# Kernel tuning notes

Hardware: AMD Instinct MI355X
Metric: run time of the kernel (lower is better)

## Reference

```python
import jax, jax.numpy as jnp
import numpy as np

N, E, D, H = 50000, 800000, 128, 8
HD = D // H  # head dim = 16


def setup_inputs() -> dict:
    key = jax.random.key(0)
    ks = jax.random.split(key, 9)
    x = jax.random.normal(ks[0], (N, D), dtype=jnp.float32)
    edge_index = jax.random.randint(ks[1], (2, E), 0, N, dtype=jnp.int64)
    s = 0.05
    Wq = jax.random.normal(ks[2], (D, D), dtype=jnp.float32) * s
    bq = jax.random.normal(ks[3], (D,), dtype=jnp.float32) * s
    Wk = jax.random.normal(ks[4], (D, D), dtype=jnp.float32) * s
    bk = jax.random.normal(ks[5], (D,), dtype=jnp.float32) * s
    Wv = jax.random.normal(ks[6], (D, D), dtype=jnp.float32) * s
    bv = jax.random.normal(ks[7], (D,), dtype=jnp.float32) * s
    return {"x": x, "Wq": Wq, "bq": bq, "Wk": Wk, "bk": bk, "Wv": Wv, "bv": bv,
            "edge_index": edge_index}


def reference(x, Wq, bq, Wk, bk, Wv, bv, edge_index):
    n = x.shape[0]
    # Linear projections (torch Linear: x @ W.T + b), split into heads
    Q = (x @ Wq.T + bq).reshape(n, H, HD)  # [N,H,hd]
    K = (x @ Wk.T + bk).reshape(n, H, HD)
    V = (x @ Wv.T + bv).reshape(n, H, HD)
    src, dst = edge_index[0], edge_index[1]
    # per-edge attention score: sum over head dim of K[src]*Q[dst]/sqrt(hd), clamp, exp
    score = jnp.sum(K[src] * Q[dst], axis=-1, keepdims=True) / np.sqrt(HD)  # [E,H,1]
    score = jnp.exp(jnp.clip(score, -5.0, 5.0))
    msg = V[src] * score  # [E,H,hd]
    wV = jax.ops.segment_sum(msg, dst, num_segments=n)      # [N,H,hd]
    Z = jax.ops.segment_sum(score, dst, num_segments=n)     # [N,H,1]
    h_out = wV / (Z + 1e-6)
    return h_out.reshape(n, H * HD)
```

## Files before the change

### kernel.cpp

```cpp
#include <hip/hip_runtime.h>
#include <hip/hip_bf16.h>

#define NN 50000
#define EE 800000
#define DD 128
#define HH 8
#define CAP 64
#define KVS 256
#define QB 391
#define PAB 196
#define NBIN 196
#define RSTRIDE 4096

typedef short bf16x8 __attribute__((ext_vector_type(8)));
typedef float f32x4 __attribute__((ext_vector_type(4)));
typedef unsigned short ushort8_t __attribute__((ext_vector_type(8)));

__device__ __forceinline__ unsigned short f2b(float f) {
    unsigned int u = __builtin_bit_cast(unsigned int, f);
    unsigned int r = (u + 0x7FFFu + ((u >> 16) & 1u)) >> 16;
    return (unsigned short)r;
}
__device__ __forceinline__ float b2f(unsigned short u) {
    return __builtin_bit_cast(float, ((unsigned int)u) << 16);
}

__global__ __launch_bounds__(256) void prep(const float* __restrict__ Wq,
                                            const float* __restrict__ Wk,
                                            const float* __restrict__ Wv,
                                            unsigned short* __restrict__ Wqb,
                                            unsigned short* __restrict__ Wkb,
                                            unsigned short* __restrict__ Wvb) {
    int idx = blockIdx.x * 256 + threadIdx.x;
    int mat = idx >> 12;
    int off = idx & 4095;
    const float* src = (mat == 0) ? Wq : (mat == 1) ? Wk : Wv;
    unsigned short* dst = (mat == 0) ? Wqb : (mat == 1) ? Wkb : Wvb;
    float4 v = ((const float4*)src)[off];
    ushort4 o;
    o.x = f2b(v.x); o.y = f2b(v.y); o.z = f2b(v.z); o.w = f2b(v.w);
    ((ushort4*)dst)[off] = o;
}

template <int OUTKIND>
__device__ __forceinline__ void qkv_mat(const unsigned short* __restrict__ W,
                                        const float* __restrict__ bias,
                                        float* __restrict__ qo,
                                        unsigned short* __restrict__ kvo,
                                        int kvoff,
                                        const bf16x8 a[2][4],
                                        int r0, int mrow, int kb,
                                        bool act0, bool act1) {
#pragma unroll
    for (int c0 = 0; c0 < 8; ++c0) {
        float bval = bias[c0 * 16 + mrow];
        const unsigned short* wr = W + (size_t)(c0 * 16 + mrow) * DD + kb * 8;
        bf16x8 w0 = *(const bf16x8*)(wr);
        bf16x8 w1 = *(const bf16x8*)(wr + 32);
        bf16x8 w2 = *(const bf16x8*)(wr + 64);
        bf16x8 w3 = *(const bf16x8*)(wr + 96);
#pragma unroll
        for (int g = 0; g < 2; ++g) {
            bool act = (g == 0) ? act0 : act1;
            f32x4 acc = {bval, bval, bval, bval};
            acc = __builtin_amdgcn_mfma_f32_16x16x32_bf16(a[g][0], w0, acc, 0, 0, 0);
            acc = __builtin_amdgcn_mfma_f32_16x16x32_bf16(a[g][1], w1, acc, 0, 0, 0);
            acc = __builtin_amdgcn_mfma_f32_16x16x32_bf16(a[g][2], w2, acc, 0, 0, 0);
            acc = __builtin_amdgcn_mfma_f32_16x16x32_bf16(a[g][3], w3, acc, 0, 0, 0);
            if (act) {
                int orow = r0 + 16 * g + kb * 4;
                int col = c0 * 16 + mrow;
                if (OUTKIND == 0) {
#pragma unroll
                    for (int r = 0; r < 4; ++r)
                        qo[(size_t)(orow + r) * DD + col] = acc[r];
                } else {
#pragma unroll
                    for (int r = 0; r < 4; ++r)
                        kvo[(size_t)(orow + r) * KVS + kvoff + col] = f2b(acc[r]);
                }
            }
        }
    }
}

__global__ __launch_bounds__(256) void mega(
    const float* __restrict__ x,
    const unsigned short* __restrict__ Wq, const float* __restrict__ bq,
    const unsigned short* __restrict__ Wk, const float* __restrict__ bk,
    const unsigned short* __restrict__ Wv, const float* __restrict__ bv,
    const int* __restrict__ ei,
    float* __restrict__ Qo, unsigned short* __restrict__ KV,
    int2* __restrict__ runbuf, int* __restrict__ gcount,
    int* __restrict__ gstart) {
    __shared__ int lcnt[256];
    __shared__ int lpre[256];
    if (blockIdx.x < QB) {
        const int wave = threadIdx.x >> 6;
        const int l = threadIdx.x & 63;
        const int r0 = blockIdx.x * 128 + wave * 32;
        const int mrow = l & 15;
        const int kb = l >> 4;
        const bool act0 = (r0 < NN);
        const bool act1 = (r0 + 16 < NN);
        if (!act0) return;

        bf16x8 a[2][4];
#pragma unroll
        for (int g = 0; g < 2; ++g) {
            int row = (g == 0 || act1) ? (r0 + 16 * g + mrow) : r0;
            const float* xr = x + (size_t)row * DD + kb * 8;
#pragma unroll
            for (int s = 0; s < 4; ++s) {
                float4 f0 = *(const float4*)(xr + s * 32);
                float4 f1 = *(const float4*)(xr + s * 32 + 4);
                bf16x8 t;
                t[0] = (short)f2b(f0.x); t[1] = (short)f2b(f0.y);
                t[2] = (short)f2b(f0.z); t[3] = (short)f2b(f0.w);
                t[4] = (short)f2b(f1.x); t[5] = (short)f2b(f1.y);
                t[6] = (short)f2b(f1.z); t[7] = (short)f2b(f1.w);
                a[g][s] = t;
            }
        }
        qkv_mat<0>(Wq, bq, Qo, (unsigned short*)nullptr, 0, a, r0, mrow, kb, act0, act1);
        qkv_mat<1>(Wk, bk, (float*)nullptr, KV, 0,   a, r0, mrow, kb, act0, act1);
        qkv_mat<1>(Wv, bv, (float*)nullptr, KV, 128, a, r0, mrow, kb, act0, act1);
    } else {
        const int b = blockIdx.x - QB;
        const int t = threadIdx.x;
        lcnt[t] = 0;
        __syncthreads();

        int ss[16], dd[16], slot[16];
        int base4 = b * 1024 + t;
#pragma unroll
        for (int j = 0; j < 4; ++j) {
            int idx = base4 + j * 256;
            int4 sv = make_int4(0, 0, 0, 0);
            int4 dv = make_int4(-1, -1, -1, -1);
            if (idx < EE / 4) {
                sv = ((const int4*)ei)[idx];
                dv = ((const int4*)(ei + EE))[idx];
            }
            ss[j * 4 + 0] = sv.x; ss[j * 4 + 1] = sv.y;
            ss[j * 4 + 2] = sv.z; ss[j * 4 + 3] = sv.w;
            dd[j * 4 + 0] = dv.x; dd[j * 4 + 1] = dv.y;
            dd[j * 4 + 2] = dv.z; dd[j * 4 + 3] = dv.w;
        }
#pragma unroll
        for (int k = 0; k < 16; ++k)
            slot[k] = (dd[k] >= 0) ? atomicAdd(&lcnt[dd[k] >> 8], 1) : 0;
        __syncthreads();

        int myCnt = lcnt[t];
        lpre[t] = myCnt;
        __syncthreads();
        for (int off = 1; off < 256; off <<= 1) {
            int v = (t >= off) ? lpre[t - off] : 0;
            __syncthreads();
            lpre[t] += v;
            __syncthreads();
        }
        int excl = lpre[t] - myCnt;
        __syncthreads();
        lpre[t] = excl;
        __syncthreads();

#pragma unroll
        for (int k = 0; k < 16; ++k) {
            if (dd[k] >= 0) {
                int pos = b * RSTRIDE + lpre[dd[k] >> 8] + slot[k];
                runbuf[pos] = make_int2(ss[k], dd[k]);
            }
        }
        if (t < NBIN) {
            gcount[t * PAB + b] = myCnt;
            gstart[t * PAB + b] = excl;
        }
    }
}

__global__ __launch_bounds__(256) void binscatter(const int2* __restrict__ runbuf,
                                                  const int* __restrict__ gcount,
                                                  const int* __restrict__ gstart,
                                                  int* __restrict__ cnt,
                                                  int* __restrict__ bucket) {
    __shared__ int cnt2[256];
    const int c = blockIdx.x, t = threadIdx.x;
    cnt2[t] = 0;
    __syncthreads();
    if (t < PAB) {
        int start = gstart[c * PAB + t];
        int count = gcount[c * PAB + t];
        const int2* run = runbuf + t * RSTRIDE + start;
        for (int i = 0; i < count; ++i) {
            int2 e = run[i];
            int p = atomicAdd(&cnt2[e.y & 255], 1);
            if (p < CAP) bucket[e.y * CAP + p] = e.x;
        }
    }
    __syncthreads();
    int node = c * 256 + t;
    if (node < NN) cnt[node] = cnt2[t];
}

__global__ __launch_bounds__(256) void gather4(const unsigned short* __restrict__ KV,
                                               const int* __restrict__ cnt,
                                               const int* __restrict__ bucket,
                                               float* __restrict__ qout) {
    int n = blockIdx.x * 4 + (threadIdx.x >> 6);
    if (n >= NN) return;
    int l = threadIdx.x & 63;
    int es = l >> 4;
    int q = l & 15;

    const float4* qrow = (const float4*)(qout + (size_t)n * DD + 8 * q);
    float4 qa = qrow[0], qb = qrow[1];
    float4 acca = make_float4(0.f, 0.f, 0.f, 0.f);
    float4 accb = make_float4(0.f, 0.f, 0.f, 0.f);
    float z = 0.f;
    int d = min(cnt[n], CAP);
    int mySrc = (l < d) ? bucket[n * CAP + l] : 0;

    for (int i = 0; i < d; i += 4) {
        int eidx = i + es;
        bool valid = eidx < d;
        int src = __shfl(mySrc, valid ? eidx : i);
        const unsigned short* kr = KV + (size_t)src * KVS + 8 * q;
        ushort8_t ku = *(const ushort8_t*)kr;
        ushort8_t vu = *(const ushort8_t*)(kr + 128);
        float s = qa.x * b2f(ku[0]) + qa.y * b2f(ku[1]) +
                  qa.z * b2f(ku[2]) + qa.w * b2f(ku[3]) +
                  qb.x * b2f(ku[4]) + qb.y * b2f(ku[5]) +
                  qb.z * b2f(ku[6]) + qb.w * b2f(ku[7]);
        s += __shfl_xor(s, 1);
        s *= 0.25f;
        s = fminf(fmaxf(s, -5.f), 5.f);
        s = __expf(s);
        if (!valid) s = 0.f;
        acca.x += b2f(vu[0]) * s; acca.y += b2f(vu[1]) * s;
        acca.z += b2f(vu[2]) * s; acca.w += b2f(vu[3]) * s;
        accb.x += b2f(vu[4]) * s; accb.y += b2f(vu[5]) * s;
        accb.z += b2f(vu[6]) * s; accb.w += b2f(vu[7]) * s;
        z += s;
    }
#pragma unroll
    for (int m = 16; m <= 32; m <<= 1) {
        acca.x += __shfl_xor(acca.x, m); acca.y += __shfl_xor(acca.y, m);
        acca.z += __shfl_xor(acca.z, m); acca.w += __shfl_xor(acca.w, m);
        accb.x += __shfl_xor(accb.x, m); accb.y += __shfl_xor(accb.y, m);
        accb.z += __shfl_xor(accb.z, m); accb.w += __shfl_xor(accb.w, m);
        z += __shfl_xor(z, m);
    }
    if (es == 0) {
        float inv = 1.f / (z + 1e-6f);
        float4* orow = (float4*)(qout + (size_t)n * DD + 8 * q);
        orow[0] = make_float4(acca.x * inv, acca.y * inv, acca.z * inv, acca.w * inv);
        orow[1] = make_float4(accb.x * inv, accb.y * inv, accb.z * inv, accb.w * inv);
    }
}

extern "C" void kernel_launch(void* const* d_in, const int* in_sizes, int n_in,
                              void* d_out, int out_size, void* d_ws, size_t ws_size,
                              hipStream_t stream) {
    const float* x  = (const float*)d_in[0];
    const float* Wq = (const float*)d_in[1];
    const float* bq = (const float*)d_in[2];
    const float* Wk = (const float*)d_in[3];
    const float* bk = (const float*)d_in[4];
    const float* Wv = (const float*)d_in[5];
    const float* bv = (const float*)d_in[6];
    const int*   ei = (const int*)d_in[7];
    float* out = (float*)d_out;

    unsigned short* KV  = (unsigned short*)d_ws;
    unsigned short* Wqb = KV + (size_t)NN * KVS;
    unsigned short* Wkb = Wqb + DD * DD;
    unsigned short* Wvb = Wkb + DD * DD;
    int* cnt    = (int*)(Wvb + DD * DD);
    int* bucket = cnt + NN;
    int2* runbuf = (int2*)(bucket + (size_t)NN * CAP);
    int* gcount = (int*)(runbuf + (size_t)PAB * RSTRIDE);
    int* gstart = gcount + NBIN * PAB;

    prep<<<48, 256, 0, stream>>>(Wq, Wk, Wv, Wqb, Wkb, Wvb);
    mega<<<QB + PAB, 256, 0, stream>>>(x, Wqb, bq, Wkb, bk, Wvb, bv, ei,
                                       out, KV, runbuf, gcount, gstart);
    binscatter<<<NBIN, 256, 0, stream>>>(runbuf, gcount, gstart, cnt, bucket);
    gather4<<<(NN + 3) / 4, 256, 0, stream>>>(KV, cnt, bucket, out);
}
```

Before: 120.4 us.

## Pack edge run buffers to 32/16-bit and process 8 edges per gather step

Edge runs are packed into one int each (16-bit src plus 8-bit local dst), and buckets store 16-bit source ids. This halves the scatter-stage traffic. The gather kernel now gives each lane a full 16-wide head and processes 8 edges per wave iteration instead of 4, which removes the intra-score shuffle and halves loop trips. In exchange it needs more registers and a longer cross-lane reduction, and it relies on node ids fitting in 16 bits.

```diff
diff --git a/kernel.cpp b/kernel.cpp
--- a/kernel.cpp
+++ b/kernel.cpp
@@ -91,7 +91,7 @@
     const unsigned short* __restrict__ Wv, const float* __restrict__ bv,
     const int* __restrict__ ei,
     float* __restrict__ Qo, unsigned short* __restrict__ KV,
-    int2* __restrict__ runbuf, int* __restrict__ gcount,
+    int* __restrict__ runbuf, int* __restrict__ gcount,
     int* __restrict__ gstart) {
     __shared__ int lcnt[256];
     __shared__ int lpre[256];
@@ -170,7 +170,7 @@
         for (int k = 0; k < 16; ++k) {
             if (dd[k] >= 0) {
                 int pos = b * RSTRIDE + lpre[dd[k] >> 8] + slot[k];
-                runbuf[pos] = make_int2(ss[k], dd[k]);
+                runbuf[pos] = ss[k] | ((dd[k] & 255) << 16);
             }
         }
         if (t < NBIN) {
@@ -180,11 +180,11 @@
     }
 }
 
-__global__ __launch_bounds__(256) void binscatter(const int2* __restrict__ runbuf,
+__global__ __launch_bounds__(256) void binscatter(const int* __restrict__ runbuf,
                                                   const int* __restrict__ gcount,
                                                   const int* __restrict__ gstart,
                                                   int* __restrict__ cnt,
-                                                  int* __restrict__ bucket) {
+                                                  unsigned short* __restrict__ bucket) {
     __shared__ int cnt2[256];
     const int c = blockIdx.x, t = threadIdx.x;
     cnt2[t] = 0;
@@ -192,11 +192,13 @@
     if (t < PAB) {
         int start = gstart[c * PAB + t];
         int count = gcount[c * PAB + t];
-        const int2* run = runbuf + t * RSTRIDE + start;
+        const int* run = runbuf + t * RSTRIDE + start;
         for (int i = 0; i < count; ++i) {
-            int2 e = run[i];
-            int p = atomicAdd(&cnt2[e.y & 255], 1);
-            if (p < CAP) bucket[e.y * CAP + p] = e.x;
+            int e = run[i];
+            int dloc = (e >> 16) & 255;
+            int p = atomicAdd(&cnt2[dloc], 1);
+            if (p < CAP)
+                bucket[(size_t)(c * 256 + dloc) * CAP + p] = (unsigned short)(e & 0xFFFF);
         }
     }
     __syncthreads();
@@ -204,59 +206,69 @@
     if (node < NN) cnt[node] = cnt2[t];
 }
 
-__global__ __launch_bounds__(256) void gather4(const unsigned short* __restrict__ KV,
+__global__ __launch_bounds__(256) void gather8(const unsigned short* __restrict__ KV,
                                                const int* __restrict__ cnt,
-                                               const int* __restrict__ bucket,
+                                               const unsigned short* __restrict__ bucket,
                                                float* __restrict__ qout) {
     int n = blockIdx.x * 4 + (threadIdx.x >> 6);
     if (n >= NN) return;
     int l = threadIdx.x & 63;
-    int es = l >> 4;
-    int q = l & 15;
-
-    const float4* qrow = (const float4*)(qout + (size_t)n * DD + 8 * q);
-    float4 qa = qrow[0], qb = qrow[1];
-    float4 acca = make_float4(0.f, 0.f, 0.f, 0.f);
-    float4 accb = make_float4(0.f, 0.f, 0.f, 0.f);
+    int es = l >> 3;
+    int h = l & 7;
+
+    const float4* qp = (const float4*)(qout + (size_t)n * DD + 16 * h);
+    float4 q0 = qp[0], q1 = qp[1], q2 = qp[2], q3 = qp[3];
+    float qf[16] = {q0.x, q0.y, q0.z, q0.w, q1.x, q1.y, q1.z, q1.w,
+                    q2.x, q2.y, q2.z, q2.w, q3.x, q3.y, q3.z, q3.w};
+
+    float acc[16];
+#pragma unroll
+    for (int j = 0; j < 16; ++j) acc[j] = 0.f;
     float z = 0.f;
+
     int d = min(cnt[n], CAP);
-    int mySrc = (l < d) ? bucket[n * CAP + l] : 0;
-
-    for (int i = 0; i < d; i += 4) {
+    int mySrc = (l < d) ? (int)bucket[(size_t)n * CAP + l] : 0;
+
+    for (int i = 0; i < d; i += 8) {
         int eidx = i + es;
         bool valid = eidx < d;
         int src = __shfl(mySrc, valid ? eidx : i);
-        const unsigned short* kr = KV + (size_t)src * KVS + 8 * q;
-        ushort8_t ku = *(const ushort8_t*)kr;
-        ushort8_t vu = *(const ushort8_t*)(kr + 128);
-        float s = qa.x * b2f(ku[0]) + qa.y * b2f(ku[1]) +
-                  qa.z * b2f(ku[2]) + qa.w * b2f(ku[3]) +
-                  qb.x * b2f(ku[4]) + qb.y * b2f(ku[5]) +
-                  qb.z * b2f(ku[6]) + qb.w * b2f(ku[7]);
-        s += __shfl_xor(s, 1);
+        const unsigned short* kr = KV + (size_t)src * KVS + 16 * h;
+        ushort8_t k0 = *(const ushort8_t*)kr;
+        ushort8_t k1 = *(const ushort8_t*)(kr + 8);
+        ushort8_t v0 = *(const ushort8_t*)(kr + 128);
+        ushort8_t v1 = *(const ushort8_t*)(kr + 136);
+        float s = qf[0] * b2f(k0[0]) + qf[1] * b2f(k0[1]) +
+                  qf[2] * b2f(k0[2]) + qf[3] * b2f(k0[3]) +
+                  qf[4] * b2f(k0[4]) + qf[5] * b2f(k0[5]) +
+                  qf[6] * b2f(k0[6]) + qf[7] * b2f(k0[7]) +
+                  qf[8] * b2f(k1[0]) + qf[9] * b2f(k1[1]) +
+                  qf[10] * b2f(k1[2]) + qf[11] * b2f(k1[3]) +
+                  qf[12] * b2f(k1[4]) + qf[13] * b2f(k1[5]) +
+                  qf[14] * b2f(k1[6]) + qf[15] * b2f(k1[7]);
         s *= 0.25f;
         s = fminf(fmaxf(s, -5.f), 5.f);
         s = __expf(s);
         if (!valid) s = 0.f;
-        acca.x += b2f(vu[0]) * s; acca.y += b2f(vu[1]) * s;
-        acca.z += b2f(vu[2]) * s; acca.w += b2f(vu[3]) * s;
-        accb.x += b2f(vu[4]) * s; accb.y += b2f(vu[5]) * s;
-        accb.z += b2f(vu[6]) * s; accb.w += b2f(vu[7]) * s;
+#pragma unroll
+        for (int j = 0; j < 8; ++j) acc[j] += b2f(v0[j]) * s;
+#pragma unroll
+        for (int j = 0; j < 8; ++j) acc[8 + j] += b2f(v1[j]) * s;
         z += s;
     }
 #pragma unroll
-    for (int m = 16; m <= 32; m <<= 1) {
-        acca.x += __shfl_xor(acca.x, m); acca.y += __shfl_xor(acca.y, m);
-        acca.z += __shfl_xor(acca.z, m); acca.w += __shfl_xor(acca.w, m);
-        accb.x += __shfl_xor(accb.x, m); accb.y += __shfl_xor(accb.y, m);
-        accb.z += __shfl_xor(accb.z, m); accb.w += __shfl_xor(accb.w, m);
+    for (int m = 8; m <= 32; m <<= 1) {
+#pragma unroll
+        for (int j = 0; j < 16; ++j) acc[j] += __shfl_xor(acc[j], m);
         z += __shfl_xor(z, m);
     }
     if (es == 0) {
         float inv = 1.f / (z + 1e-6f);
-        float4* orow = (float4*)(qout + (size_t)n * DD + 8 * q);
-        orow[0] = make_float4(acca.x * inv, acca.y * inv, acca.z * inv, acca.w * inv);
-        orow[1] = make_float4(accb.x * inv, accb.y * inv, accb.z * inv, accb.w * inv);
+        float4* orow = (float4*)(qout + (size_t)n * DD + 16 * h);
+#pragma unroll
+        for (int j = 0; j < 4; ++j)
+            orow[j] = make_float4(acc[4 * j] * inv, acc[4 * j + 1] * inv,
+                                  acc[4 * j + 2] * inv, acc[4 * j + 3] * inv);
     }
 }
 
@@ -277,15 +289,15 @@
     unsigned short* Wqb = KV + (size_t)NN * KVS;
     unsigned short* Wkb = Wqb + DD * DD;
     unsigned short* Wvb = Wkb + DD * DD;
-    int* cnt    = (int*)(Wvb + DD * DD);
-    int* bucket = cnt + NN;
-    int2* runbuf = (int2*)(bucket + (size_t)NN * CAP);
-    int* gcount = (int*)(runbuf + (size_t)PAB * RSTRIDE);
+    int* cnt = (int*)(Wvb + DD * DD);
+    unsigned short* bucket = (unsigned short*)(cnt + NN);
+    int* runbuf = (int*)(bucket + (size_t)NN * CAP);
+    int* gcount = runbuf + (size_t)PAB * RSTRIDE;
     int* gstart = gcount + NBIN * PAB;
 
     prep<<<48, 256, 0, stream>>>(Wq, Wk, Wv, Wqb, Wkb, Wvb);
     mega<<<QB + PAB, 256, 0, stream>>>(x, Wqb, bq, Wkb, bk, Wvb, bv, ei,
                                        out, KV, runbuf, gcount, gstart);
     binscatter<<<NBIN, 256, 0, stream>>>(runbuf, gcount, gstart, cnt, bucket);
-    gather4<<<(NN + 3) / 4, 256, 0, stream>>>(KV, cnt, bucket, out);
-}
+    gather8<<<(NN + 3) / 4, 256, 0, stream>>>(KV, cnt, bucket, out);
+}
```

After: 119.0 us. About the same (-1.2%).
